# Performance work log

Hardware: AMD Instinct MI355X
Metric: run time of the kernel (lower is better)

The kernel has to match this reference:

```python
import jax, jax.numpy as jnp
import numpy as np

DIM = 1024
NUM_HEADS = 16
HEAD_DIM = DIM // NUM_HEADS
SCALING = float(np.sqrt(HEAD_DIM))
LN_EPS = 1e-5
B, S = 2, 2048


def setup_inputs() -> dict:
    key = jax.random.key(0)
    ks = jax.random.split(key, 4)
    x = jax.random.normal(ks[0], (B, S, DIM), dtype=jnp.float32)
    mask = jnp.zeros((B, 1, 1, S), dtype=jnp.float32)
    w_qkv = jax.random.normal(ks[1], (DIM, 3 * DIM), dtype=jnp.float32) * (1.0 / np.sqrt(DIM))
    b_qkv = jnp.zeros((3 * DIM,), dtype=jnp.float32)
    w_out = jax.random.normal(ks[2], (DIM, DIM), dtype=jnp.float32) * (1.0 / np.sqrt(DIM))
    b_out = jnp.zeros((DIM,), dtype=jnp.float32)
    ln_g = jnp.ones((DIM,), dtype=jnp.float32)
    ln_b = jnp.zeros((DIM,), dtype=jnp.float32)
    return {"x": x, "mask": mask, "w_qkv": w_qkv, "b_qkv": b_qkv,
            "w_out": w_out, "b_out": b_out, "ln_g": ln_g, "ln_b": ln_b}


def reference(x, mask, w_qkv, b_qkv, w_out, b_out, ln_g, ln_b):
    Bx, Sx, _ = x.shape
    # interleaved QKV: last-axis stride-3 split, matching torch reshape (B,S,dim,3)
    qkv = (x @ w_qkv + b_qkv).reshape(Bx, Sx, DIM, 3)
    q = qkv[..., 0]
    k = qkv[..., 1]
    v = jax.nn.elu(qkv[..., 2])
    # split heads -> (B,S,H,hd)
    q = q.reshape(Bx, Sx, NUM_HEADS, HEAD_DIM)
    k = k.reshape(Bx, Sx, NUM_HEADS, HEAD_DIM)
    v = v.reshape(Bx, Sx, NUM_HEADS, HEAD_DIM)
    scores = jnp.einsum('bqhd,bkhd->bhqk', q, k) / SCALING + mask
    attn = jax.nn.softmax(scores, axis=-1)
    out = jnp.einsum('bhqk,bkhd->bqhd', attn, v).reshape(Bx, Sx, DIM)
    out = out @ w_out + b_out
    mu = jnp.mean(out, axis=-1, keepdims=True)
    var = jnp.mean((out - mu) ** 2, axis=-1, keepdims=True)
    out = (out - mu) * jax.lax.rsqrt(var + LN_EPS) * ln_g + ln_b
    out = jax.nn.elu(out)  # Dropout in eval mode = identity
    return out + x
```

## Files before the change

### kernel.cpp

```cpp
#include <hip/hip_runtime.h>
#include <hip/hip_bf16.h>
#include <math.h>

typedef unsigned short u16;
typedef __attribute__((ext_vector_type(8))) short bf16x8;
typedef __attribute__((ext_vector_type(4))) float f32x4;

#define S_LEN 2048
#define H_CNT 16
#define HDIM 64
#define D_MODEL 1024
#define M_ROWS 4096
#define N_QKV 3072
#define LOG2E 1.4426950408889634f
#define QSCALE 0.18033688011111243f

__device__ __forceinline__ u16 f2bf(float x) {
  unsigned u = __float_as_uint(x);
  unsigned r = u + 0x7FFF + ((u >> 16) & 1);
  return (u16)(r >> 16);
}
__device__ __forceinline__ float elu_f(float v) { return v > 0.f ? v : __expf(v) - 1.f; }

__device__ __forceinline__ void gload_lds16(const void* g, void* l) {
  __builtin_amdgcn_global_load_lds((const __attribute__((address_space(1))) void*)g,
                                   (__attribute__((address_space(3))) void*)l, 16, 0, 0);
}

__global__ __launch_bounds__(256) void k_cvt(const float* __restrict__ in, u16* __restrict__ out, int n8) {
  int i = blockIdx.x * 256 + threadIdx.x;
  if (i >= n8) return;
  const float4* v = (const float4*)in;
  float4 a = v[2 * i], b = v[2 * i + 1];
  float f[8] = {a.x, a.y, a.z, a.w, b.x, b.y, b.z, b.w};
  union { u16 us[8]; bf16x8 v8; } p;
#pragma unroll
  for (int j = 0; j < 8; ++j) p.us[j] = f2bf(f[j]);
  ((bf16x8*)out)[i] = p.v8;
}

__global__ __launch_bounds__(256) void k_transpose(const float* __restrict__ in, u16* __restrict__ out,
                                                   int K, int N, int perm) {
  __shared__ float tile[32][33];
  int nb = blockIdx.x * 32, kb = blockIdx.y * 32;
#pragma unroll
  for (int r = threadIdx.y; r < 32; r += 8)
    tile[r][threadIdx.x] = in[(size_t)(kb + r) * N + nb + threadIdx.x];
  __syncthreads();
#pragma unroll
  for (int r = threadIdx.y; r < 32; r += 8) {
    int n = nb + r;
    int np = perm ? (n % 3) * (N / 3) + n / 3 : n;
    out[(size_t)np * K + kb + threadIdx.x] = f2bf(tile[threadIdx.x][r]);
  }
}

__global__ __launch_bounds__(256, 4) void k_gemm_qkv(const u16* __restrict__ A, const u16* __restrict__ Bt,
                                                     const float* __restrict__ bias3,
                                                     u16* __restrict__ Qb, u16* __restrict__ Kb,
                                                     u16* __restrict__ Vt) {
  __shared__ __align__(16) u16 sA[128 * 64];
  __shared__ __align__(16) u16 sB[64 * 64];
  const int t = threadIdx.x, lane = t & 63, wave = t >> 6;
  const int g = lane >> 4, q = lane & 15;
  const int row0 = blockIdx.x * 128, col0 = blockIdx.y * 64;

  const int srow8 = lane >> 3, scol = (lane & 7) * 8;
  const u16* gA = A + (size_t)(row0 + wave * 32 + srow8) * D_MODEL + scol;
  const u16* gB = Bt + (size_t)(col0 + wave * 16 + srow8) * D_MODEL + scol;
  u16* lA = sA + wave * 32 * 64;
  u16* lB = sB + wave * 16 * 64;

  f32x4 acc[2][4] = {};

  for (int ks = 0; ks < 16; ++ks) {
    const int ko = ks * 64;
#pragma unroll
    for (int j = 0; j < 4; ++j) gload_lds16(gA + (size_t)j * 8 * D_MODEL + ko, lA + j * 512);
#pragma unroll
    for (int j = 0; j < 2; ++j) gload_lds16(gB + (size_t)j * 8 * D_MODEL + ko, lB + j * 512);
    __syncthreads();
#pragma unroll
    for (int kk = 0; kk < 2; ++kk) {
      bf16x8 af[2], bfr[4];
#pragma unroll
      for (int i = 0; i < 2; ++i)
        af[i] = *(const bf16x8*)&sA[(wave * 32 + i * 16 + q) * 64 + kk * 32 + g * 8];
#pragma unroll
      for (int i = 0; i < 4; ++i)
        bfr[i] = *(const bf16x8*)&sB[(i * 16 + q) * 64 + kk * 32 + g * 8];
#pragma unroll
      for (int mi = 0; mi < 2; ++mi)
#pragma unroll
        for (int ni = 0; ni < 4; ++ni)
          acc[mi][ni] = __builtin_amdgcn_mfma_f32_16x16x32_bf16(af[mi], bfr[ni], acc[mi][ni], 0, 0, 0);
    }
    __syncthreads();
  }

  const int j = col0 >> 10;
  const int dbase = col0 & 1023;
  const int h = dbase >> 6;
  if (j == 2) {
#pragma unroll
    for (int mi = 0; mi < 2; ++mi) {
      const int m0 = row0 + wave * 32 + mi * 16 + g * 4;
      const int b = m0 >> 11, s0 = m0 & 2047;
#pragma unroll
      for (int ni = 0; ni < 4; ++ni) {
        const int hd = ni * 16 + q;
        const float bv = bias3[(dbase + hd) * 3 + 2];
        u16 w0 = f2bf(elu_f(acc[mi][ni][0] + bv));
        u16 w1 = f2bf(elu_f(acc[mi][ni][1] + bv));
        u16 w2 = f2bf(elu_f(acc[mi][ni][2] + bv));
        u16 w3 = f2bf(elu_f(acc[mi][ni][3] + bv));
        uint2 pk;
        pk.x = (unsigned)w0 | ((unsigned)w1 << 16);
        pk.y = (unsigned)w2 | ((unsigned)w3 << 16);
        *(uint2*)&Vt[((size_t)(b * H_CNT + h) * HDIM + hd) * S_LEN + s0] = pk;
      }
    }
  } else {
    u16* dst = j ? Kb : Qb;
    const float qs = j ? 1.f : QSCALE;
#pragma unroll
    for (int mi = 0; mi < 2; ++mi) {
      const int m0 = row0 + wave * 32 + mi * 16 + g * 4;
      const int b = m0 >> 11, s0 = m0 & 2047;
      u16* dbh = dst + (size_t)(b * H_CNT + h) * S_LEN * HDIM;
#pragma unroll
      for (int ni = 0; ni < 4; ++ni) {
        const int hd = ni * 16 + q;
        const float bv = bias3[(dbase + hd) * 3 + j];
#pragma unroll
        for (int r = 0; r < 4; ++r)
          dbh[(size_t)(s0 + r) * HDIM + hd] = f2bf((acc[mi][ni][r] + bv) * qs);
      }
    }
  }
}

__global__ __launch_bounds__(256, 4) void k_gemm_out(const u16* __restrict__ A, const u16* __restrict__ Bt,
                                                     const float* __restrict__ bias, float* __restrict__ Co) {
  __shared__ __align__(16) u16 sA[64 * 64];
  __shared__ __align__(16) u16 sB[64 * 64];
  const int t = threadIdx.x, lane = t & 63, wave = t >> 6;
  const int g = lane >> 4, q = lane & 15;
  const int wm = wave >> 1, wn = wave & 1;
  const int row0 = blockIdx.x * 64, col0 = blockIdx.y * 64;

  const int srow8 = lane >> 3, scol = (lane & 7) * 8;
  const u16* gA = A + (size_t)(row0 + wave * 16 + srow8) * D_MODEL + scol;
  const u16* gB = Bt + (size_t)(col0 + wave * 16 + srow8) * D_MODEL + scol;
  u16* lA = sA + wave * 16 * 64;
  u16* lB = sB + wave * 16 * 64;

  f32x4 acc[2][2] = {};

  for (int ks = 0; ks < 16; ++ks) {
    const int ko = ks * 64;
#pragma unroll
    for (int j = 0; j < 2; ++j) {
      gload_lds16(gA + (size_t)j * 8 * D_MODEL + ko, lA + j * 512);
      gload_lds16(gB + (size_t)j * 8 * D_MODEL + ko, lB + j * 512);
    }
    __syncthreads();
#pragma unroll
    for (int kk = 0; kk < 2; ++kk) {
      bf16x8 af[2], bfr[2];
#pragma unroll
      for (int i = 0; i < 2; ++i) {
        af[i] = *(const bf16x8*)&sA[(wm * 32 + i * 16 + q) * 64 + kk * 32 + g * 8];
        bfr[i] = *(const bf16x8*)&sB[(wn * 32 + i * 16 + q) * 64 + kk * 32 + g * 8];
      }
#pragma unroll
      for (int mi = 0; mi < 2; ++mi)
#pragma unroll
        for (int ni = 0; ni < 2; ++ni)
          acc[mi][ni] = __builtin_amdgcn_mfma_f32_16x16x32_bf16(af[mi], bfr[ni], acc[mi][ni], 0, 0, 0);
    }
    __syncthreads();
  }

#pragma unroll
  for (int mi = 0; mi < 2; ++mi) {
    const int m0 = row0 + wm * 32 + mi * 16 + g * 4;
#pragma unroll
    for (int ni = 0; ni < 2; ++ni) {
      const int c = col0 + wn * 32 + ni * 16 + q;
      const float bv = bias[c];
#pragma unroll
      for (int r = 0; r < 4; ++r) Co[(size_t)(m0 + r) * D_MODEL + c] = acc[mi][ni][r] + bv;
    }
  }
}

__global__ __launch_bounds__(256, 4) void k_attn(const u16* __restrict__ Qb, const u16* __restrict__ Kb,
                                                 const u16* __restrict__ Vt, const float* __restrict__ mask,
                                                 u16* __restrict__ Ob) {
  __shared__ __align__(16) u16 sK[2][64 * 64];
  __shared__ __align__(16) u16 sV[2][64 * 64];
  __shared__ __align__(16) u16 pl[4][16 * 64];
  const int t = threadIdx.x, lane = t & 63, wave = t >> 6;
  const int g = lane >> 4, q = lane & 15;
  const int qt = blockIdx.x, bh = blockIdx.y;
  const int b = bh >> 4, h = bh & 15;
  const u16* Qp = Qb + (size_t)bh * S_LEN * HDIM;
  const u16* Kp = Kb + (size_t)bh * S_LEN * HDIM;
  const u16* Vp = Vt + (size_t)bh * HDIM * S_LEN;
  const float* mp = mask + (size_t)b * S_LEN;

  const int srow = lane >> 3;
  const int scol = ((lane & 7) ^ srow) * 8;
  const u16* gK = Kp + (size_t)(wave * 8 + srow) * HDIM + scol;
  const u16* gV = Vp + (size_t)(wave * 8 + srow) * S_LEN + scol;

  const int qrow = qt * 64 + wave * 16 + q;
  bf16x8 qf[2];
  qf[0] = *(const bf16x8*)&Qp[(size_t)qrow * HDIM + g * 8];
  qf[1] = *(const bf16x8*)&Qp[(size_t)qrow * HDIM + 32 + g * 8];

  f32x4 o[4] = {};
  float lpart = 0.f;
  const f32x4 minit = {-8.f, -8.f, -8.f, -8.f};

#define STG(KV, BUF)                                          \
  do {                                                        \
    const u16* gk_ = gK + (size_t)(KV) * HDIM;                \
    const u16* gv_ = gV + (KV);                               \
    u16* lk_ = &sK[BUF][wave * 8 * 64];                       \
    u16* lv_ = &sV[BUF][wave * 8 * 64];                       \
    gload_lds16(gk_, lk_);                                    \
    gload_lds16(gk_ + 32 * HDIM, lk_ + 32 * 64);              \
    gload_lds16(gv_, lv_);                                    \
    gload_lds16(gv_ + 32 * S_LEN, lv_ + 32 * 64);             \
  } while (0)

#define STEP(IT, CB, NB, DOSTG)                                                          \
  do {                                                                                   \
    const int kv = (IT) * 64;                                                            \
    if (DOSTG) STG(kv + 64, NB);                                                         \
    const u16* kb = &sK[CB][0];                                                          \
    const u16* vb = &sV[CB][0];                                                          \
    f32x4 sacc[4] = {minit, minit, minit, minit};                                        \
    __builtin_amdgcn_s_setprio(1);                                                       \
    _Pragma("unroll") for (int c = 0; c < 4; ++c) {                                      \
      bf16x8 kf0 = *(const bf16x8*)&kb[(c * 16 + q) * 64 + ((g ^ (q & 7)) * 8)];         \
      bf16x8 kf1 = *(const bf16x8*)&kb[(c * 16 + q) * 64 + (((4 + g) ^ (q & 7)) * 8)];   \
      sacc[c] = __builtin_amdgcn_mfma_f32_16x16x32_bf16(kf0, qf[0], sacc[c], 0, 0, 0);   \
      sacc[c] = __builtin_amdgcn_mfma_f32_16x16x32_bf16(kf1, qf[1], sacc[c], 0, 0, 0);   \
    }                                                                                    \
    __builtin_amdgcn_s_setprio(0);                                                       \
    float p[4][4];                                                                       \
    _Pragma("unroll") for (int c = 0; c < 4; ++c) {                                      \
      float4 mk = *(const float4*)&mp[kv + c * 16 + g * 4];                              \
      p[c][0] = __builtin_amdgcn_exp2f(fmaf(mk.x, LOG2E, sacc[c][0]));                   \
      p[c][1] = __builtin_amdgcn_exp2f(fmaf(mk.y, LOG2E, sacc[c][1]));                   \
      p[c][2] = __builtin_amdgcn_exp2f(fmaf(mk.z, LOG2E, sacc[c][2]));                   \
      p[c][3] = __builtin_amdgcn_exp2f(fmaf(mk.w, LOG2E, sacc[c][3]));                   \
      lpart += (p[c][0] + p[c][1]) + (p[c][2] + p[c][3]);                                \
    }                                                                                    \
    char* plw = (char*)&pl[wave][0];                                                     \
    _Pragma("unroll") for (int c = 0; c < 4; ++c) {                                      \
      unsigned d0, d1;                                                                   \
      asm("v_cvt_pk_bf16_f32 %0, %1, %2" : "=v"(d0) : "v"(p[c][0]), "v"(p[c][1]));       \
      asm("v_cvt_pk_bf16_f32 %0, %1, %2" : "=v"(d1) : "v"(p[c][2]), "v"(p[c][3]));       \
      *(uint2*)(plw + q * 128 + (((unsigned)(c * 32 + g * 8)) ^ ((unsigned)(q & 7) << 4))) = \
          make_uint2(d0, d1);                                                            \
    }                                                                                    \
    bf16x8 pa0 = *(const bf16x8*)(plw + q * 128 + (((unsigned)(g * 16)) ^ ((unsigned)(q & 7) << 4)));       \
    bf16x8 pa1 = *(const bf16x8*)(plw + q * 128 + (((unsigned)(64 + g * 16)) ^ ((unsigned)(q & 7) << 4)));  \
    __builtin_amdgcn_s_setprio(1);                                                       \
    _Pragma("unroll") for (int nf = 0; nf < 4; ++nf) {                                   \
      bf16x8 vf0 = *(const bf16x8*)&vb[(nf * 16 + q) * 64 + ((g ^ (q & 7)) * 8)];        \
      o[nf] = __builtin_amdgcn_mfma_f32_16x16x32_bf16(pa0, vf0, o[nf], 0, 0, 0);         \
    }                                                                                    \
    _Pragma("unroll") for (int nf = 0; nf < 4; ++nf) {                                   \
      bf16x8 vf1 = *(const bf16x8*)&vb[(nf * 16 + q) * 64 + (((4 + g) ^ (q & 7)) * 8)];  \
      o[nf] = __builtin_amdgcn_mfma_f32_16x16x32_bf16(pa1, vf1, o[nf], 0, 0, 0);         \
    }                                                                                    \
    __builtin_amdgcn_s_setprio(0);                                                       \
    __syncthreads();                                                                     \
  } while (0)

  STG(0, 0);
  __syncthreads();

  for (int it2 = 0; it2 < S_LEN / 128; ++it2) {
    STEP(2 * it2, 0, 1, 1);
    STEP(2 * it2 + 1, 1, 0, it2 < S_LEN / 128 - 1);
  }
#undef STEP
#undef STG

  lpart += __shfl_xor(lpart, 16);
  lpart += __shfl_xor(lpart, 32);
  const float inv = 1.f / lpart;
  float iv[4];
#pragma unroll
  for (int r = 0; r < 4; ++r) iv[r] = __shfl(inv, g * 4 + r);
  const int orow0 = b * S_LEN + qt * 64 + wave * 16 + g * 4;
#pragma unroll
  for (int r = 0; r < 4; ++r) {
    const size_t base = (size_t)(orow0 + r) * D_MODEL + h * HDIM + q;
#pragma unroll
    for (int nf = 0; nf < 4; ++nf) Ob[base + nf * 16] = f2bf(o[nf][r] * iv[r]);
  }
}

__global__ __launch_bounds__(256) void k_ln(float* __restrict__ po, const float* __restrict__ x,
                                            const float* __restrict__ g, const float* __restrict__ bb) {
  const int row = blockIdx.x, t = threadIdx.x;
  float4 v = ((const float4*)(po + (size_t)row * D_MODEL))[t];
  float s = v.x + v.y + v.z + v.w;
  float s2 = v.x * v.x + v.y * v.y + v.z * v.z + v.w * v.w;
#pragma unroll
  for (int m = 1; m < 64; m <<= 1) {
    s += __shfl_xor(s, m);
    s2 += __shfl_xor(s2, m);
  }
  __shared__ float rs[4], rs2[4];
  if ((t & 63) == 0) {
    rs[t >> 6] = s;
    rs2[t >> 6] = s2;
  }
  __syncthreads();
  s = rs[0] + rs[1] + rs[2] + rs[3];
  s2 = rs2[0] + rs2[1] + rs2[2] + rs2[3];
  const float mean = s * (1.f / 1024.f);
  const float var = s2 * (1.f / 1024.f) - mean * mean;
  const float rstd = rsqrtf(var + 1e-5f);
  float4 xg = ((const float4*)(x + (size_t)row * D_MODEL))[t];
  float4 gg = ((const float4*)g)[t];
  float4 bv = ((const float4*)bb)[t];
  float4 o;
  o.x = elu_f((v.x - mean) * rstd * gg.x + bv.x) + xg.x;
  o.y = elu_f((v.y - mean) * rstd * gg.y + bv.y) + xg.y;
  o.z = elu_f((v.z - mean) * rstd * gg.z + bv.z) + xg.z;
  o.w = elu_f((v.w - mean) * rstd * gg.w + bv.w) + xg.w;
  ((float4*)(po + (size_t)row * D_MODEL))[t] = o;
}

extern "C" void kernel_launch(void* const* d_in, const int* in_sizes, int n_in, void* d_out,
                              int out_size, void* d_ws, size_t ws_size, hipStream_t stream) {
  const float* x = (const float*)d_in[0];
  const float* mask = (const float*)d_in[1];
  const float* w_qkv = (const float*)d_in[2];
  const float* b_qkv = (const float*)d_in[3];
  const float* w_out = (const float*)d_in[4];
  const float* b_out = (const float*)d_in[5];
  const float* ln_g = (const float*)d_in[6];
  const float* ln_b = (const float*)d_in[7];
  float* out = (float*)d_out;

  char* ws = (char*)d_ws;
  u16* xb = (u16*)(ws);
  u16* wqkvT = (u16*)(ws + (8ull << 20));
  u16* woutT = (u16*)(ws + (14ull << 20));
  u16* Qb = (u16*)(ws + (16ull << 20));
  u16* Kb = (u16*)(ws + (24ull << 20));
  u16* Vt = (u16*)(ws + (32ull << 20));
  u16* Ob = (u16*)(ws + (40ull << 20));

  k_cvt<<<2048, 256, 0, stream>>>(x, xb, (M_ROWS * D_MODEL) / 8);
  dim3 tb(32, 8);
  k_transpose<<<dim3(N_QKV / 32, D_MODEL / 32), tb, 0, stream>>>(w_qkv, wqkvT, D_MODEL, N_QKV, 1);
  k_transpose<<<dim3(D_MODEL / 32, D_MODEL / 32), tb, 0, stream>>>(w_out, woutT, D_MODEL, D_MODEL, 0);
  k_gemm_qkv<<<dim3(M_ROWS / 128, N_QKV / 64), 256, 0, stream>>>(xb, wqkvT, b_qkv, Qb, Kb, Vt);
  k_attn<<<dim3(S_LEN / 64, 32), 256, 0, stream>>>(Qb, Kb, Vt, mask, Ob);
  k_gemm_out<<<dim3(M_ROWS / 64, D_MODEL / 64), 256, 0, stream>>>(Ob, woutT, b_out, out);
  k_ln<<<M_ROWS, 256, 0, stream>>>(out, x, ln_g, ln_b);
}
```

Baseline: 144.6 us.

## Process two query sub-tiles per wave in attention with 128-thread blocks

```diff
diff --git a/kernel.cpp b/kernel.cpp
--- a/kernel.cpp
+++ b/kernel.cpp
@@ -195,12 +195,12 @@
   }
 }
 
-__global__ __launch_bounds__(256, 4) void k_attn(const u16* __restrict__ Qb, const u16* __restrict__ Kb,
+__global__ __launch_bounds__(128, 3) void k_attn(const u16* __restrict__ Qb, const u16* __restrict__ Kb,
                                                  const u16* __restrict__ Vt, const float* __restrict__ mask,
                                                  u16* __restrict__ Ob) {
   __shared__ __align__(16) u16 sK[2][64 * 64];
   __shared__ __align__(16) u16 sV[2][64 * 64];
-  __shared__ __align__(16) u16 pl[4][16 * 64];
+  __shared__ __align__(16) u16 pl[2][2][16 * 64];
   const int t = threadIdx.x, lane = t & 63, wave = t >> 6;
   const int g = lane >> 4, q = lane & 15;
   const int qt = blockIdx.x, bh = blockIdx.y;
@@ -212,28 +212,28 @@
 
   const int srow = lane >> 3;
   const int scol = ((lane & 7) ^ srow) * 8;
-  const u16* gK = Kp + (size_t)(wave * 8 + srow) * HDIM + scol;
-  const u16* gV = Vp + (size_t)(wave * 8 + srow) * S_LEN + scol;
-
-  const int qrow = qt * 64 + wave * 16 + q;
-  bf16x8 qf[2];
-  qf[0] = *(const bf16x8*)&Qp[(size_t)qrow * HDIM + g * 8];
-  qf[1] = *(const bf16x8*)&Qp[(size_t)qrow * HDIM + 32 + g * 8];
-
-  f32x4 o[4] = {};
-  float lpart = 0.f;
+  const u16* gK = Kp + (size_t)(wave * 32 + srow) * HDIM + scol;
+  const u16* gV = Vp + (size_t)(wave * 32 + srow) * S_LEN + scol;
+
+  const int qr0 = qt * 64 + wave * 32 + q;
+  bf16x8 qf[2][2];
+  qf[0][0] = *(const bf16x8*)&Qp[(size_t)qr0 * HDIM + g * 8];
+  qf[0][1] = *(const bf16x8*)&Qp[(size_t)qr0 * HDIM + 32 + g * 8];
+  qf[1][0] = *(const bf16x8*)&Qp[(size_t)(qr0 + 16) * HDIM + g * 8];
+  qf[1][1] = *(const bf16x8*)&Qp[(size_t)(qr0 + 16) * HDIM + 32 + g * 8];
+
+  f32x4 o[2][4] = {};
+  float lpart[2] = {0.f, 0.f};
   const f32x4 minit = {-8.f, -8.f, -8.f, -8.f};
 
-#define STG(KV, BUF)                                          \
-  do {                                                        \
-    const u16* gk_ = gK + (size_t)(KV) * HDIM;                \
-    const u16* gv_ = gV + (KV);                               \
-    u16* lk_ = &sK[BUF][wave * 8 * 64];                       \
-    u16* lv_ = &sV[BUF][wave * 8 * 64];                       \
-    gload_lds16(gk_, lk_);                                    \
-    gload_lds16(gk_ + 32 * HDIM, lk_ + 32 * 64);              \
-    gload_lds16(gv_, lv_);                                    \
-    gload_lds16(gv_ + 32 * S_LEN, lv_ + 32 * 64);             \
+#define STG(KV, BUF)                                                             \
+  do {                                                                           \
+    const u16* gk_ = gK + (size_t)(KV)*HDIM;                                     \
+    const u16* gv_ = gV + (KV);                                                  \
+    _Pragma("unroll") for (int j_ = 0; j_ < 4; ++j_) {                           \
+      gload_lds16(gk_ + (size_t)j_ * 8 * HDIM, &sK[BUF][(wave * 32 + j_ * 8) * 64]);  \
+      gload_lds16(gv_ + (size_t)j_ * 8 * S_LEN, &sV[BUF][(wave * 32 + j_ * 8) * 64]); \
+    }                                                                            \
   } while (0)
 
 #define STEP(IT, CB, NB, DOSTG)                                                          \
@@ -242,42 +242,51 @@
     if (DOSTG) STG(kv + 64, NB);                                                         \
     const u16* kb = &sK[CB][0];                                                          \
     const u16* vb = &sV[CB][0];                                                          \
-    f32x4 sacc[4] = {minit, minit, minit, minit};                                        \
+    f32x4 sacc[2][4] = {{minit, minit, minit, minit}, {minit, minit, minit, minit}};     \
     __builtin_amdgcn_s_setprio(1);                                                       \
     _Pragma("unroll") for (int c = 0; c < 4; ++c) {                                      \
       bf16x8 kf0 = *(const bf16x8*)&kb[(c * 16 + q) * 64 + ((g ^ (q & 7)) * 8)];         \
       bf16x8 kf1 = *(const bf16x8*)&kb[(c * 16 + q) * 64 + (((4 + g) ^ (q & 7)) * 8)];   \
-      sacc[c] = __builtin_amdgcn_mfma_f32_16x16x32_bf16(kf0, qf[0], sacc[c], 0, 0, 0);   \
-      sacc[c] = __builtin_amdgcn_mfma_f32_16x16x32_bf16(kf1, qf[1], sacc[c], 0, 0, 0);   \
+      sacc[0][c] = __builtin_amdgcn_mfma_f32_16x16x32_bf16(kf0, qf[0][0], sacc[0][c], 0, 0, 0); \
+      sacc[0][c] = __builtin_amdgcn_mfma_f32_16x16x32_bf16(kf1, qf[0][1], sacc[0][c], 0, 0, 0); \
+      sacc[1][c] = __builtin_amdgcn_mfma_f32_16x16x32_bf16(kf0, qf[1][0], sacc[1][c], 0, 0, 0); \
+      sacc[1][c] = __builtin_amdgcn_mfma_f32_16x16x32_bf16(kf1, qf[1][1], sacc[1][c], 0, 0, 0); \
     }                                                                                    \
     __builtin_amdgcn_s_setprio(0);                                                       \
-    float p[4][4];                                                                       \
-    _Pragma("unroll") for (int c = 0; c < 4; ++c) {                                      \
-      float4 mk = *(const float4*)&mp[kv + c * 16 + g * 4];                              \
-      p[c][0] = __builtin_amdgcn_exp2f(fmaf(mk.x, LOG2E, sacc[c][0]));                   \
-      p[c][1] = __builtin_amdgcn_exp2f(fmaf(mk.y, LOG2E, sacc[c][1]));                   \
-      p[c][2] = __builtin_amdgcn_exp2f(fmaf(mk.z, LOG2E, sacc[c][2]));                   \
-      p[c][3] = __builtin_amdgcn_exp2f(fmaf(mk.w, LOG2E, sacc[c][3]));                   \
-      lpart += (p[c][0] + p[c][1]) + (p[c][2] + p[c][3]);                                \
-    }                                                                                    \
-    char* plw = (char*)&pl[wave][0];                                                     \
-    _Pragma("unroll") for (int c = 0; c < 4; ++c) {                                      \
-      unsigned d0, d1;                                                                   \
-      asm("v_cvt_pk_bf16_f32 %0, %1, %2" : "=v"(d0) : "v"(p[c][0]), "v"(p[c][1]));       \
-      asm("v_cvt_pk_bf16_f32 %0, %1, %2" : "=v"(d1) : "v"(p[c][2]), "v"(p[c][3]));       \
-      *(uint2*)(plw + q * 128 + (((unsigned)(c * 32 + g * 8)) ^ ((unsigned)(q & 7) << 4))) = \
-          make_uint2(d0, d1);                                                            \
-    }                                                                                    \
-    bf16x8 pa0 = *(const bf16x8*)(plw + q * 128 + (((unsigned)(g * 16)) ^ ((unsigned)(q & 7) << 4)));       \
-    bf16x8 pa1 = *(const bf16x8*)(plw + q * 128 + (((unsigned)(64 + g * 16)) ^ ((unsigned)(q & 7) << 4)));  \
+    float4 mkv[4];                                                                       \
+    _Pragma("unroll") for (int c = 0; c < 4; ++c)                                        \
+        mkv[c] = *(const float4*)&mp[kv + c * 16 + g * 4];                               \
+    _Pragma("unroll") for (int qg = 0; qg < 2; ++qg) {                                   \
+      char* plw = (char*)&pl[wave][qg][0];                                               \
+      _Pragma("unroll") for (int c = 0; c < 4; ++c) {                                    \
+        float p0 = __builtin_amdgcn_exp2f(fmaf(mkv[c].x, LOG2E, sacc[qg][c][0]));        \
+        float p1 = __builtin_amdgcn_exp2f(fmaf(mkv[c].y, LOG2E, sacc[qg][c][1]));        \
+        float p2 = __builtin_amdgcn_exp2f(fmaf(mkv[c].z, LOG2E, sacc[qg][c][2]));        \
+        float p3 = __builtin_amdgcn_exp2f(fmaf(mkv[c].w, LOG2E, sacc[qg][c][3]));        \
+        lpart[qg] += (p0 + p1) + (p2 + p3);                                              \
+        unsigned d0, d1;                                                                 \
+        asm("v_cvt_pk_bf16_f32 %0, %1, %2" : "=v"(d0) : "v"(p0), "v"(p1));               \
+        asm("v_cvt_pk_bf16_f32 %0, %1, %2" : "=v"(d1) : "v"(p2), "v"(p3));               \
+        *(uint2*)(plw + q * 128 + (((unsigned)(c * 32 + g * 8)) ^ ((unsigned)(q & 7) << 4))) = \
+            make_uint2(d0, d1);                                                          \
+      }                                                                                  \
+    }                                                                                    \
+    bf16x8 pa[2][2];                                                                     \
+    _Pragma("unroll") for (int qg = 0; qg < 2; ++qg) {                                   \
+      char* plw = (char*)&pl[wave][qg][0];                                               \
+      pa[qg][0] = *(const bf16x8*)(plw + q * 128 + (((unsigned)(g * 16)) ^ ((unsigned)(q & 7) << 4)));      \
+      pa[qg][1] = *(const bf16x8*)(plw + q * 128 + (((unsigned)(64 + g * 16)) ^ ((unsigned)(q & 7) << 4))); \
+    }                                                                                    \
     __builtin_amdgcn_s_setprio(1);                                                       \
     _Pragma("unroll") for (int nf = 0; nf < 4; ++nf) {                                   \
       bf16x8 vf0 = *(const bf16x8*)&vb[(nf * 16 + q) * 64 + ((g ^ (q & 7)) * 8)];        \
-      o[nf] = __builtin_amdgcn_mfma_f32_16x16x32_bf16(pa0, vf0, o[nf], 0, 0, 0);         \
+      o[0][nf] = __builtin_amdgcn_mfma_f32_16x16x32_bf16(pa[0][0], vf0, o[0][nf], 0, 0, 0); \
+      o[1][nf] = __builtin_amdgcn_mfma_f32_16x16x32_bf16(pa[1][0], vf0, o[1][nf], 0, 0, 0); \
     }                                                                                    \
     _Pragma("unroll") for (int nf = 0; nf < 4; ++nf) {                                   \
       bf16x8 vf1 = *(const bf16x8*)&vb[(nf * 16 + q) * 64 + (((4 + g) ^ (q & 7)) * 8)];  \
-      o[nf] = __builtin_amdgcn_mfma_f32_16x16x32_bf16(pa1, vf1, o[nf], 0, 0, 0);         \
+      o[0][nf] = __builtin_amdgcn_mfma_f32_16x16x32_bf16(pa[0][1], vf1, o[0][nf], 0, 0, 0); \
+      o[1][nf] = __builtin_amdgcn_mfma_f32_16x16x32_bf16(pa[1][1], vf1, o[1][nf], 0, 0, 0); \
     }                                                                                    \
     __builtin_amdgcn_s_setprio(0);                                                       \
     __syncthreads();                                                                     \
@@ -293,18 +302,22 @@
 #undef STEP
 #undef STG
 
-  lpart += __shfl_xor(lpart, 16);
-  lpart += __shfl_xor(lpart, 32);
-  const float inv = 1.f / lpart;
-  float iv[4];
-#pragma unroll
-  for (int r = 0; r < 4; ++r) iv[r] = __shfl(inv, g * 4 + r);
-  const int orow0 = b * S_LEN + qt * 64 + wave * 16 + g * 4;
-#pragma unroll
-  for (int r = 0; r < 4; ++r) {
-    const size_t base = (size_t)(orow0 + r) * D_MODEL + h * HDIM + q;
-#pragma unroll
-    for (int nf = 0; nf < 4; ++nf) Ob[base + nf * 16] = f2bf(o[nf][r] * iv[r]);
+#pragma unroll
+  for (int qg = 0; qg < 2; ++qg) {
+    float lp = lpart[qg];
+    lp += __shfl_xor(lp, 16);
+    lp += __shfl_xor(lp, 32);
+    const float inv = 1.f / lp;
+    float iv[4];
+#pragma unroll
+    for (int r = 0; r < 4; ++r) iv[r] = __shfl(inv, g * 4 + r);
+    const int orow0 = b * S_LEN + qt * 64 + wave * 32 + qg * 16 + g * 4;
+#pragma unroll
+    for (int r = 0; r < 4; ++r) {
+      const size_t base = (size_t)(orow0 + r) * D_MODEL + h * HDIM + q;
+#pragma unroll
+      for (int nf = 0; nf < 4; ++nf) Ob[base + nf * 16] = f2bf(o[qg][nf][r] * iv[r]);
+    }
   }
 }
 
@@ -367,7 +380,7 @@
   k_transpose<<<dim3(N_QKV / 32, D_MODEL / 32), tb, 0, stream>>>(w_qkv, wqkvT, D_MODEL, N_QKV, 1);
   k_transpose<<<dim3(D_MODEL / 32, D_MODEL / 32), tb, 0, stream>>>(w_out, woutT, D_MODEL, D_MODEL, 0);
   k_gemm_qkv<<<dim3(M_ROWS / 128, N_QKV / 64), 256, 0, stream>>>(xb, wqkvT, b_qkv, Qb, Kb, Vt);
-  k_attn<<<dim3(S_LEN / 64, 32), 256, 0, stream>>>(Qb, Kb, Vt, mask, Ob);
+  k_attn<<<dim3(S_LEN / 64, 32), 128, 0, stream>>>(Qb, Kb, Vt, mask, Ob);
   k_gemm_out<<<dim3(M_ROWS / 64, D_MODEL / 64), 256, 0, stream>>>(Ob, woutT, b_out, out);
   k_ln<<<M_ROWS, 256, 0, stream>>>(out, x, ln_g, ln_b);
 }
```

Result: slower. 150.7 us (+4.2%).

## Enlarge QKV GEMM tile to 128x128 with XOR-swizzled LDS and block swizzle

Applied to the files above, without the earlier changes.

```diff
diff --git a/kernel.cpp b/kernel.cpp
--- a/kernel.cpp
+++ b/kernel.cpp
@@ -60,37 +60,43 @@
                                                      u16* __restrict__ Qb, u16* __restrict__ Kb,
                                                      u16* __restrict__ Vt) {
   __shared__ __align__(16) u16 sA[128 * 64];
-  __shared__ __align__(16) u16 sB[64 * 64];
+  __shared__ __align__(16) u16 sB[128 * 64];
   const int t = threadIdx.x, lane = t & 63, wave = t >> 6;
   const int g = lane >> 4, q = lane & 15;
-  const int row0 = blockIdx.x * 128, col0 = blockIdx.y * 64;
-
-  const int srow8 = lane >> 3, scol = (lane & 7) * 8;
+  const int wm = wave >> 1, wn = wave & 1;
+  const int bid = blockIdx.y * 32 + blockIdx.x;
+  const int swz = (bid & 7) * 96 + (bid >> 3);
+  const int row0 = (swz & 31) * 128, col0 = (swz >> 5) * 128;
+
+  const int srow8 = lane >> 3;
+  const int scol = ((lane & 7) ^ srow8) * 8;
   const u16* gA = A + (size_t)(row0 + wave * 32 + srow8) * D_MODEL + scol;
-  const u16* gB = Bt + (size_t)(col0 + wave * 16 + srow8) * D_MODEL + scol;
-  u16* lA = sA + wave * 32 * 64;
-  u16* lB = sB + wave * 16 * 64;
-
-  f32x4 acc[2][4] = {};
+  const u16* gB = Bt + (size_t)(col0 + wave * 32 + srow8) * D_MODEL + scol;
+  u16* lA = sA + wave * 2048;
+  u16* lB = sB + wave * 2048;
+
+  f32x4 acc[4][4] = {};
 
   for (int ks = 0; ks < 16; ++ks) {
     const int ko = ks * 64;
 #pragma unroll
-    for (int j = 0; j < 4; ++j) gload_lds16(gA + (size_t)j * 8 * D_MODEL + ko, lA + j * 512);
-#pragma unroll
-    for (int j = 0; j < 2; ++j) gload_lds16(gB + (size_t)j * 8 * D_MODEL + ko, lB + j * 512);
+    for (int j = 0; j < 4; ++j) {
+      gload_lds16(gA + (size_t)j * 8 * D_MODEL + ko, lA + j * 512);
+      gload_lds16(gB + (size_t)j * 8 * D_MODEL + ko, lB + j * 512);
+    }
     __syncthreads();
 #pragma unroll
     for (int kk = 0; kk < 2; ++kk) {
-      bf16x8 af[2], bfr[4];
-#pragma unroll
-      for (int i = 0; i < 2; ++i)
-        af[i] = *(const bf16x8*)&sA[(wave * 32 + i * 16 + q) * 64 + kk * 32 + g * 8];
-#pragma unroll
-      for (int i = 0; i < 4; ++i)
-        bfr[i] = *(const bf16x8*)&sB[(i * 16 + q) * 64 + kk * 32 + g * 8];
-#pragma unroll
-      for (int mi = 0; mi < 2; ++mi)
+      bf16x8 af[4], bfr[4];
+#pragma unroll
+      for (int i = 0; i < 4; ++i) {
+        af[i] = *(const bf16x8*)&sA[(wm * 64 + i * 16 + q) * 64 +
+                                    (((unsigned)(kk * 4 + g) ^ (unsigned)(q & 7)) * 8)];
+        bfr[i] = *(const bf16x8*)&sB[(wn * 64 + i * 16 + q) * 64 +
+                                     (((unsigned)(kk * 4 + g) ^ (unsigned)(q & 7)) * 8)];
+      }
+#pragma unroll
+      for (int mi = 0; mi < 4; ++mi)
 #pragma unroll
         for (int ni = 0; ni < 4; ++ni)
           acc[mi][ni] = __builtin_amdgcn_mfma_f32_16x16x32_bf16(af[mi], bfr[ni], acc[mi][ni], 0, 0, 0);
@@ -99,17 +105,16 @@
   }
 
   const int j = col0 >> 10;
-  const int dbase = col0 & 1023;
-  const int h = dbase >> 6;
   if (j == 2) {
 #pragma unroll
-    for (int mi = 0; mi < 2; ++mi) {
-      const int m0 = row0 + wave * 32 + mi * 16 + g * 4;
+    for (int mi = 0; mi < 4; ++mi) {
+      const int m0 = row0 + wm * 64 + mi * 16 + g * 4;
       const int b = m0 >> 11, s0 = m0 & 2047;
 #pragma unroll
       for (int ni = 0; ni < 4; ++ni) {
-        const int hd = ni * 16 + q;
-        const float bv = bias3[(dbase + hd) * 3 + 2];
+        const int d = (col0 & 1023) + wn * 64 + ni * 16 + q;
+        const int h = d >> 6, hd = d & 63;
+        const float bv = bias3[d * 3 + 2];
         u16 w0 = f2bf(elu_f(acc[mi][ni][0] + bv));
         u16 w1 = f2bf(elu_f(acc[mi][ni][1] + bv));
         u16 w2 = f2bf(elu_f(acc[mi][ni][2] + bv));
@@ -124,14 +129,15 @@
     u16* dst = j ? Kb : Qb;
     const float qs = j ? 1.f : QSCALE;
 #pragma unroll
-    for (int mi = 0; mi < 2; ++mi) {
-      const int m0 = row0 + wave * 32 + mi * 16 + g * 4;
+    for (int mi = 0; mi < 4; ++mi) {
+      const int m0 = row0 + wm * 64 + mi * 16 + g * 4;
       const int b = m0 >> 11, s0 = m0 & 2047;
-      u16* dbh = dst + (size_t)(b * H_CNT + h) * S_LEN * HDIM;
 #pragma unroll
       for (int ni = 0; ni < 4; ++ni) {
-        const int hd = ni * 16 + q;
-        const float bv = bias3[(dbase + hd) * 3 + j];
+        const int d = (col0 & 1023) + wn * 64 + ni * 16 + q;
+        const int h = d >> 6, hd = d & 63;
+        const float bv = bias3[d * 3 + j];
+        u16* dbh = dst + (size_t)(b * H_CNT + h) * S_LEN * HDIM;
 #pragma unroll
         for (int r = 0; r < 4; ++r)
           dbh[(size_t)(s0 + r) * HDIM + hd] = f2bf((acc[mi][ni][r] + bv) * qs);
@@ -366,7 +372,7 @@
   dim3 tb(32, 8);
   k_transpose<<<dim3(N_QKV / 32, D_MODEL / 32), tb, 0, stream>>>(w_qkv, wqkvT, D_MODEL, N_QKV, 1);
   k_transpose<<<dim3(D_MODEL / 32, D_MODEL / 32), tb, 0, stream>>>(w_out, woutT, D_MODEL, D_MODEL, 0);
-  k_gemm_qkv<<<dim3(M_ROWS / 128, N_QKV / 64), 256, 0, stream>>>(xb, wqkvT, b_qkv, Qb, Kb, Vt);
+  k_gemm_qkv<<<dim3(M_ROWS / 128, N_QKV / 128), 256, 0, stream>>>(xb, wqkvT, b_qkv, Qb, Kb, Vt);
   k_attn<<<dim3(S_LEN / 64, 32), 256, 0, stream>>>(Qb, Kb, Vt, mask, Ob);
   k_gemm_out<<<dim3(M_ROWS / 64, D_MODEL / 64), 256, 0, stream>>>(Ob, woutT, b_out, out);
   k_ln<<<M_ROWS, 256, 0, stream>>>(out, x, ln_g, ln_b);
```

Measured after the change: 139.4 us. 3.6% less time.
